# Optimization experiments

Hardware: AMD Instinct MI355X
Metric: run time of the kernel (lower is better)

## Reference

```python
import jax, jax.numpy as jnp
import numpy as np
import math

D_MODEL, HEADS, KQ = 1024, 16, 64
B, S = 2, 2048

def setup_inputs() -> dict:
    key = jax.random.key(0)
    k1, k2, k3, k4, k5 = jax.random.split(key, 5)
    scale = D_MODEL ** (-0.5)
    return {
        "x_BSE": jax.random.normal(k1, (B, S, D_MODEL), dtype=jnp.float32),
        "w_q": jax.random.normal(k2, (D_MODEL, HEADS, KQ), dtype=jnp.float32) * scale,
        "w_k": jax.random.normal(k3, (D_MODEL, HEADS, KQ), dtype=jnp.float32) * scale,
        "w_v": jax.random.normal(k4, (D_MODEL, HEADS, KQ), dtype=jnp.float32) * scale,
        "w_o": jax.random.normal(k5, (D_MODEL, HEADS, KQ), dtype=jnp.float32) * scale,
    }

def reference(x_BSE, w_q, w_k, w_v, w_o):
    # QKV projections (self-attention: memory = x)
    q_BSHK = jnp.einsum('BSE,EHK->BSHK', x_BSE, w_q)
    k_BMHK = jnp.einsum('BSE,EHK->BSHK', x_BSE, w_k)
    v_BMHK = jnp.einsum('BSE,EHK->BSHK', x_BSE, w_v)
    logits_BSHM = jnp.einsum('BSHK,BMHK->BSHM', q_BSHK, k_BMHK) / math.sqrt(KQ)
    # causal (diagonal) mask: query position >= memory position
    Sdim, Mdim = logits_BSHM.shape[1], logits_BSHM.shape[3]
    qpos = jnp.arange(Sdim)[:, None]          # [S,1]
    mpos = jnp.arange(Mdim)[None, :]          # [1,M]
    mask_SM = jnp.where(qpos >= mpos, 0.0, -jnp.inf).astype(logits_BSHM.dtype)
    logits_BSHM = logits_BSHM + mask_SM[None, :, None, :]
    probs_BSHM = jax.nn.softmax(logits_BSHM, axis=3)
    out_BSHK = jnp.einsum('BSHM,BMHK->BSHK', probs_BSHM, v_BMHK)
    return jnp.einsum('BSHK,EHK->BSE', out_BSHK, w_o)
```

## Files before the change

### kernel.cpp

```cpp
#include <hip/hip_runtime.h>
#include <hip/hip_bf16.h>

typedef __attribute__((ext_vector_type(4)))  float f32x4;
typedef __attribute__((ext_vector_type(16))) float f32x16;
typedef __attribute__((ext_vector_type(8)))  short short8;
typedef __attribute__((ext_vector_type(4)))  short short4v;

__device__ __forceinline__ short f2bf(float f) {
  union { float f; unsigned u; } x; x.f = f;
  unsigned r = (x.u + 0x7FFFu + ((x.u >> 16) & 1u)) >> 16;
  return (short)r;
}
__device__ __forceinline__ unsigned cvtpk(float lo, float hi) {
  unsigned r;
  asm("v_cvt_pk_bf16_f32 %0, %1, %2" : "=v"(r) : "v"(lo), "v"(hi));
  return r;
}

__global__ __launch_bounds__(256) void k_cast(const float* __restrict__ in,
                                              short* __restrict__ out, int n4) {
  int i = blockIdx.x * 256 + threadIdx.x;
  if (i >= n4) return;
  f32x4 v = ((const f32x4*)in)[i];
  short4v s;
  s[0] = f2bf(v[0]); s[1] = f2bf(v[1]); s[2] = f2bf(v[2]); s[3] = f2bf(v[3]);
  ((short4v*)out)[i] = s;
}

__global__ __launch_bounds__(256) void k_pack(const float* __restrict__ wq,
                                              const float* __restrict__ wk,
                                              const float* __restrict__ wv,
                                              short* __restrict__ WT) {
  int nt = blockIdx.x, et = blockIdx.y, sel = blockIdx.z;
  const float* w = sel == 0 ? wq : (sel == 1 ? wk : wv);
  __shared__ float tile[64][65];
  int tid = threadIdx.x;
  int cl = tid & 63, rw = tid >> 6;
#pragma unroll
  for (int j = 0; j < 16; ++j) {
    int el = j * 4 + rw;
    tile[el][cl] = w[(size_t)(et * 64 + el) * 1024 + nt * 64 + cl];
  }
  __syncthreads();
#pragma unroll
  for (int j = 0; j < 16; ++j) {
    int nl = j * 4 + rw;
    int n = sel * 1024 + nt * 64 + nl;
    WT[(size_t)n * 1024 + et * 64 + cl] = f2bf(tile[cl][nl]);
  }
}

template <int EPI>
__global__ __launch_bounds__(256) void k_gemm(const short* __restrict__ A,
                                              const short* __restrict__ B,
                                              short* __restrict__ Qo, short* __restrict__ Ko,
                                              short* __restrict__ Vo, float* __restrict__ out,
                                              int M, int N, int K) {
  __shared__ short As[128][40];
  __shared__ short Bs[128][40];
  int tid = threadIdx.x;
  int bm = blockIdx.y * 128, bn = blockIdx.x * 128;
  int wid = tid >> 6, lane = tid & 63;
  int wm = (wid >> 1) * 64, wn = (wid & 1) * 64;
  int lg = lane >> 4, lr = lane & 15;
  f32x4 acc[4][4] = {};

  int sr = tid >> 2, sc = tid & 3;
  const short* Ar0 = A + (size_t)(bm + sr) * K;
  const short* Ar1 = A + (size_t)(bm + sr + 64) * K;
  const short* Br0 = B + (size_t)(bn + sr) * K;
  const short* Br1 = B + (size_t)(bn + sr + 64) * K;

  short8 pa0 = *(const short8*)&Ar0[sc * 8];
  short8 pa1 = *(const short8*)&Ar1[sc * 8];
  short8 pb0 = *(const short8*)&Br0[sc * 8];
  short8 pb1 = *(const short8*)&Br1[sc * 8];

  int nk = K >> 5;
  for (int kt = 0; kt < nk; ++kt) {
    __syncthreads();
    *(short8*)&As[sr][sc * 8] = pa0;
    *(short8*)&As[sr + 64][sc * 8] = pa1;
    *(short8*)&Bs[sr][sc * 8] = pb0;
    *(short8*)&Bs[sr + 64][sc * 8] = pb1;
    if (kt + 1 < nk) {
      int ko = (kt + 1) * 32;
      pa0 = *(const short8*)&Ar0[ko + sc * 8];
      pa1 = *(const short8*)&Ar1[ko + sc * 8];
      pb0 = *(const short8*)&Br0[ko + sc * 8];
      pb1 = *(const short8*)&Br1[ko + sc * 8];
    }
    __syncthreads();
    short8 af[4], bf_[4];
#pragma unroll
    for (int mt = 0; mt < 4; ++mt)
      af[mt] = *(const short8*)&As[wm + mt * 16 + lr][lg * 8];
#pragma unroll
    for (int ntl = 0; ntl < 4; ++ntl)
      bf_[ntl] = *(const short8*)&Bs[wn + ntl * 16 + lr][lg * 8];
#pragma unroll
    for (int mt = 0; mt < 4; ++mt)
#pragma unroll
      for (int ntl = 0; ntl < 4; ++ntl)
        acc[mt][ntl] = __builtin_amdgcn_mfma_f32_16x16x32_bf16(af[mt], bf_[ntl], acc[mt][ntl], 0, 0, 0);
  }

#pragma unroll
  for (int mt = 0; mt < 4; ++mt)
#pragma unroll
    for (int ntl = 0; ntl < 4; ++ntl) {
      int m0 = bm + wm + mt * 16 + lg * 4;
      int n = bn + wn + ntl * 16 + lr;
      if (EPI == 0) {
        int b = m0 >> 11, s0 = m0 & 2047;
        int sel = n >> 10, hk = n & 1023;
        int h = hk >> 6, kd = hk & 63;
        if (sel == 0) {
#pragma unroll
          for (int rr = 0; rr < 4; ++rr)
            Qo[((size_t)(b * 16 + h) * 2048 + s0 + rr) * 64 + kd] =
                f2bf(acc[mt][ntl][rr] * 0.18033688011112042f);
        } else if (sel == 1) {
#pragma unroll
          for (int rr = 0; rr < 4; ++rr)
            Ko[((size_t)(b * 16 + h) * 2048 + s0 + rr) * 64 + kd] = f2bf(acc[mt][ntl][rr]);
        } else {
          short4v v4;
#pragma unroll
          for (int rr = 0; rr < 4; ++rr) v4[rr] = f2bf(acc[mt][ntl][rr]);
          *(short4v*)&Vo[((size_t)(b * 16 + h) * 64 + kd) * 2048 + s0] = v4;
        }
      } else {
#pragma unroll
        for (int rr = 0; rr < 4; ++rr)
          out[(size_t)(m0 + rr) * 1024 + n] = acc[mt][ntl][rr];
      }
    }
}

__global__ __launch_bounds__(128, 2) void k_attn(const short* __restrict__ Q,
                                                 const short* __restrict__ K,
                                                 const short* __restrict__ VT,
                                                 short* __restrict__ O) {
  const int S = 2048;
  int bh = blockIdx.x;
  int g = 31 - blockIdx.y;

  int tid = threadIdx.x;
  int wid = tid >> 6, lane = tid & 63;
  int hi = lane >> 5, ln = lane & 31;
  int qw = 2 * g + wid;
  int q_g = qw * 32 + ln;
  int npair = g + 1;

  __shared__ short Ks[2][2][32][64];
  __shared__ short Vs[2][2][64][32];

  const short* Qb = Q + (size_t)bh * S * 64;
  const short* Kb = K + (size_t)bh * S * 64;
  const short* Vb = VT + (size_t)bh * 64 * S;

  short8 qf[4];
#pragma unroll
  for (int ds = 0; ds < 4; ++ds)
    qf[ds] = *(const short8*)&Qb[(size_t)q_g * 64 + ds * 16 + hi * 8];

  int kr = tid >> 2, kcb = tid & 3;
  int vd = tid >> 1, vcb = tid & 1;
  const short* kgp = Kb + (size_t)kr * 64;
  const short* vgp = Vb + (size_t)vd * S;

  short8 ka0 = *(const short8*)&kgp[kcb * 8];
  short8 ka1 = *(const short8*)&kgp[(kcb + 4) * 8];
  short8 kb0 = *(const short8*)&kgp[2048 + kcb * 8];
  short8 kb1 = *(const short8*)&kgp[2048 + (kcb + 4) * 8];
  short8 va0 = *(const short8*)&vgp[vcb * 8];
  short8 va1 = *(const short8*)&vgp[(vcb + 2) * 8];
  short8 vb0 = *(const short8*)&vgp[32 + vcb * 8];
  short8 vb1 = *(const short8*)&vgp[32 + (vcb + 2) * 8];

  f32x16 acoA = {}, acoB = {};
  float l = 0.f;

  for (int p = 0; p < npair; ++p) {
    int pb = p & 1;
    *(short8*)&Ks[pb][0][kr][(kcb ^ (kr & 7)) * 8]       = ka0;
    *(short8*)&Ks[pb][0][kr][((kcb + 4) ^ (kr & 7)) * 8] = ka1;
    *(short8*)&Ks[pb][1][kr][(kcb ^ (kr & 7)) * 8]       = kb0;
    *(short8*)&Ks[pb][1][kr][((kcb + 4) ^ (kr & 7)) * 8] = kb1;
    *(short8*)&Vs[pb][0][vd][(vcb ^ (vd & 3)) * 8]       = va0;
    *(short8*)&Vs[pb][0][vd][((vcb + 2) ^ (vd & 3)) * 8] = va1;
    *(short8*)&Vs[pb][1][vd][(vcb ^ (vd & 3)) * 8]       = vb0;
    *(short8*)&Vs[pb][1][vd][((vcb + 2) ^ (vd & 3)) * 8] = vb1;
    if (p + 1 < npair) {
      size_t ko0 = (size_t)(2 * p + 2) * 2048, ko1 = (size_t)(2 * p + 3) * 2048;
      size_t vo0 = (size_t)(2 * p + 2) * 32,   vo1 = (size_t)(2 * p + 3) * 32;
      ka0 = *(const short8*)&kgp[ko0 + kcb * 8];
      ka1 = *(const short8*)&kgp[ko0 + (kcb + 4) * 8];
      kb0 = *(const short8*)&kgp[ko1 + kcb * 8];
      kb1 = *(const short8*)&kgp[ko1 + (kcb + 4) * 8];
      va0 = *(const short8*)&vgp[vo0 + vcb * 8];
      va1 = *(const short8*)&vgp[vo0 + (vcb + 2) * 8];
      vb0 = *(const short8*)&vgp[vo1 + vcb * 8];
      vb1 = *(const short8*)&vgp[vo1 + (vcb + 2) * 8];
    }
    __syncthreads();

    int t0 = 2 * p, t1 = 2 * p + 1;

    short8 kc00 = *(const short8*)&Ks[pb][0][ln][((0 + hi) ^ (ln & 7)) * 8];
    short8 kc01 = *(const short8*)&Ks[pb][0][ln][((2 + hi) ^ (ln & 7)) * 8];
    short8 kc02 = *(const short8*)&Ks[pb][0][ln][((4 + hi) ^ (ln & 7)) * 8];
    short8 kc03 = *(const short8*)&Ks[pb][0][ln][((6 + hi) ^ (ln & 7)) * 8];
    short8 kc10 = *(const short8*)&Ks[pb][1][ln][((0 + hi) ^ (ln & 7)) * 8];
    short8 kc11 = *(const short8*)&Ks[pb][1][ln][((2 + hi) ^ (ln & 7)) * 8];
    short8 kc12 = *(const short8*)&Ks[pb][1][ln][((4 + hi) ^ (ln & 7)) * 8];
    short8 kc13 = *(const short8*)&Ks[pb][1][ln][((6 + hi) ^ (ln & 7)) * 8];

    f32x16 sa0 = {}, sa1 = {};
    __builtin_amdgcn_s_setprio(1);
    sa0 = __builtin_amdgcn_mfma_f32_32x32x16_bf16(kc00, qf[0], sa0, 0, 0, 0);
    sa1 = __builtin_amdgcn_mfma_f32_32x32x16_bf16(kc10, qf[0], sa1, 0, 0, 0);
    sa0 = __builtin_amdgcn_mfma_f32_32x32x16_bf16(kc01, qf[1], sa0, 0, 0, 0);
    sa1 = __builtin_amdgcn_mfma_f32_32x32x16_bf16(kc11, qf[1], sa1, 0, 0, 0);
    sa0 = __builtin_amdgcn_mfma_f32_32x32x16_bf16(kc02, qf[2], sa0, 0, 0, 0);
    sa1 = __builtin_amdgcn_mfma_f32_32x32x16_bf16(kc12, qf[2], sa1, 0, 0, 0);
    sa0 = __builtin_amdgcn_mfma_f32_32x32x16_bf16(kc03, qf[3], sa0, 0, 0, 0);
    sa1 = __builtin_amdgcn_mfma_f32_32x32x16_bf16(kc13, qf[3], sa1, 0, 0, 0);
    __builtin_amdgcn_s_setprio(0);

    if (t0 >= qw) {
#pragma unroll
      for (int r = 0; r < 16; ++r) {
        int kv_g = t0 * 32 + (r & 3) + 8 * (r >> 2) + 4 * hi;
        if (kv_g > q_g) sa0[r] = -1e30f;
      }
    }
    if (t1 >= qw) {
#pragma unroll
      for (int r = 0; r < 16; ++r) {
        int kv_g = t1 * 32 + (r & 3) + 8 * (r >> 2) + 4 * hi;
        if (kv_g > q_g) sa1[r] = -1e30f;
      }
    }

    float p0[16], p1[16];
#pragma unroll
    for (int r = 0; r < 16; ++r) p0[r] = exp2f(sa0[r]);
#pragma unroll
    for (int r = 0; r < 16; ++r) p1[r] = exp2f(sa1[r]);
    {
      float s00 = (p0[0] + p0[1]) + (p0[2] + p0[3]);
      float s01 = (p0[4] + p0[5]) + (p0[6] + p0[7]);
      float s02 = (p0[8] + p0[9]) + (p0[10] + p0[11]);
      float s03 = (p0[12] + p0[13]) + (p0[14] + p0[15]);
      float s10 = (p1[0] + p1[1]) + (p1[2] + p1[3]);
      float s11 = (p1[4] + p1[5]) + (p1[6] + p1[7]);
      float s12 = (p1[8] + p1[9]) + (p1[10] + p1[11]);
      float s13 = (p1[12] + p1[13]) + (p1[14] + p1[15]);
      l += ((s00 + s01) + (s02 + s03)) + ((s10 + s11) + (s12 + s13));
    }

    {
      short8 v00 = *(const short8*)&Vs[pb][0][ln][((0 + hi) ^ (ln & 3)) * 8];
      short8 v01 = *(const short8*)&Vs[pb][0][ln][((2 + hi) ^ (ln & 3)) * 8];
      short8 v10 = *(const short8*)&Vs[pb][0][32 + ln][((0 + hi) ^ (ln & 3)) * 8];
      short8 v11 = *(const short8*)&Vs[pb][0][32 + ln][((2 + hi) ^ (ln & 3)) * 8];
#pragma unroll
      for (int s = 0; s < 2; ++s) {
        unsigned c0 = cvtpk(p0[8 * s + 0], p0[8 * s + 1]);
        unsigned c1 = cvtpk(p0[8 * s + 2], p0[8 * s + 3]);
        unsigned c2 = cvtpk(p0[8 * s + 4], p0[8 * s + 5]);
        unsigned c3 = cvtpk(p0[8 * s + 6], p0[8 * s + 7]);
        unsigned r1 = (unsigned)__shfl_xor((int)(hi ? c0 : c2), 32);
        unsigned r2 = (unsigned)__shfl_xor((int)(hi ? c1 : c3), 32);
        union { unsigned u[4]; short8 v; } pbv;
        pbv.u[0] = hi ? r1 : c0;
        pbv.u[1] = hi ? r2 : c1;
        pbv.u[2] = hi ? c2 : r1;
        pbv.u[3] = hi ? c3 : r2;
        __builtin_amdgcn_s_setprio(1);
        if (s == 0) {
          acoA = __builtin_amdgcn_mfma_f32_32x32x16_bf16(v00, pbv.v, acoA, 0, 0, 0);
          acoB = __builtin_amdgcn_mfma_f32_32x32x16_bf16(v10, pbv.v, acoB, 0, 0, 0);
        } else {
          acoA = __builtin_amdgcn_mfma_f32_32x32x16_bf16(v01, pbv.v, acoA, 0, 0, 0);
          acoB = __builtin_amdgcn_mfma_f32_32x32x16_bf16(v11, pbv.v, acoB, 0, 0, 0);
        }
        __builtin_amdgcn_s_setprio(0);
      }
    }
    {
      short8 v00 = *(const short8*)&Vs[pb][1][ln][((0 + hi) ^ (ln & 3)) * 8];
      short8 v01 = *(const short8*)&Vs[pb][1][ln][((2 + hi) ^ (ln & 3)) * 8];
      short8 v10 = *(const short8*)&Vs[pb][1][32 + ln][((0 + hi) ^ (ln & 3)) * 8];
      short8 v11 = *(const short8*)&Vs[pb][1][32 + ln][((2 + hi) ^ (ln & 3)) * 8];
#pragma unroll
      for (int s = 0; s < 2; ++s) {
        unsigned c0 = cvtpk(p1[8 * s + 0], p1[8 * s + 1]);
        unsigned c1 = cvtpk(p1[8 * s + 2], p1[8 * s + 3]);
        unsigned c2 = cvtpk(p1[8 * s + 4], p1[8 * s + 5]);
        unsigned c3 = cvtpk(p1[8 * s + 6], p1[8 * s + 7]);
        unsigned r1 = (unsigned)__shfl_xor((int)(hi ? c0 : c2), 32);
        unsigned r2 = (unsigned)__shfl_xor((int)(hi ? c1 : c3), 32);
        union { unsigned u[4]; short8 v; } pbv;
        pbv.u[0] = hi ? r1 : c0;
        pbv.u[1] = hi ? r2 : c1;
        pbv.u[2] = hi ? c2 : r1;
        pbv.u[3] = hi ? c3 : r2;
        __builtin_amdgcn_s_setprio(1);
        if (s == 0) {
          acoA = __builtin_amdgcn_mfma_f32_32x32x16_bf16(v00, pbv.v, acoA, 0, 0, 0);
          acoB = __builtin_amdgcn_mfma_f32_32x32x16_bf16(v10, pbv.v, acoB, 0, 0, 0);
        } else {
          acoA = __builtin_amdgcn_mfma_f32_32x32x16_bf16(v01, pbv.v, acoA, 0, 0, 0);
          acoB = __builtin_amdgcn_mfma_f32_32x32x16_bf16(v11, pbv.v, acoB, 0, 0, 0);
        }
        __builtin_amdgcn_s_setprio(0);
      }
    }
  }

  l += __shfl_xor(l, 32);
  float rl = 1.f / l;
  int b = bh >> 4, h = bh & 15;
  size_t obase = ((size_t)b * 2048 + q_g) * 1024 + h * 64;
#pragma unroll
  for (int g4 = 0; g4 < 4; ++g4) {
    int d0 = 8 * g4 + 4 * hi;
    *(unsigned*)&O[obase + d0]          = cvtpk(acoA[4 * g4] * rl, acoA[4 * g4 + 1] * rl);
    *(unsigned*)&O[obase + d0 + 2]      = cvtpk(acoA[4 * g4 + 2] * rl, acoA[4 * g4 + 3] * rl);
    *(unsigned*)&O[obase + 32 + d0]     = cvtpk(acoB[4 * g4] * rl, acoB[4 * g4 + 1] * rl);
    *(unsigned*)&O[obase + 32 + d0 + 2] = cvtpk(acoB[4 * g4 + 2] * rl, acoB[4 * g4 + 3] * rl);
  }
}

extern "C" void kernel_launch(void* const* d_in, const int* in_sizes, int n_in,
                              void* d_out, int out_size, void* d_ws, size_t ws_size,
                              hipStream_t stream) {
  const float* x  = (const float*)d_in[0];
  const float* wq = (const float*)d_in[1];
  const float* wk = (const float*)d_in[2];
  const float* wv = (const float*)d_in[3];
  const float* wo = (const float*)d_in[4];
  float* out = (float*)d_out;
  char* ws = (char*)d_ws;

  short* x_bf  = (short*)(ws);
  short* WqkvT = (short*)(ws + ((size_t)8 << 20));
  short* wo_bf = (short*)(ws + ((size_t)14 << 20));
  short* Qb    = (short*)(ws + ((size_t)16 << 20));
  short* Kb    = (short*)(ws + ((size_t)24 << 20));
  short* Vt    = (short*)(ws + ((size_t)32 << 20));
  short* Ob    = (short*)(ws + ((size_t)40 << 20));

  k_cast<<<4096, 256, 0, stream>>>(x, x_bf, 1048576);
  k_cast<<<1024, 256, 0, stream>>>(wo, wo_bf, 262144);
  k_pack<<<dim3(16, 16, 3), 256, 0, stream>>>(wq, wk, wv, WqkvT);
  k_gemm<0><<<dim3(24, 32), 256, 0, stream>>>(x_bf, WqkvT, Qb, Kb, Vt, nullptr, 4096, 3072, 1024);
  k_attn<<<dim3(32, 32), 128, 0, stream>>>(Qb, Kb, Vt, Ob);
  k_gemm<1><<<dim3(8, 32), 256, 0, stream>>>(Ob, wo_bf, nullptr, nullptr, nullptr, out, 4096, 1024, 1024);
}
```

Measured before the change: 124.7 us.

## Process two query tiles per attention wave to reuse staged K/V tiles

Each attention block now covers 128 query rows instead of 64, with each wave handling two 32-row query tiles that share the same K/V tiles in LDS. This halves the grid in y and halves global K/V traffic and LDS staging per query, and it hoists the V fragment reads out so both query sets use them. It also rewrites the P permutation to use four lane shuffles instead of two selected ones. In exchange the kernel uses more registers (two sets of accumulators and Q fragments), launches fewer blocks, and gives the diagonal block some masked work that is wasted.

```diff
diff --git a/kernel.cpp b/kernel.cpp
--- a/kernel.cpp
+++ b/kernel.cpp
@@ -144,14 +144,16 @@
                                                  short* __restrict__ O) {
   const int S = 2048;
   int bh = blockIdx.x;
-  int g = 31 - blockIdx.y;
+  int g = 15 - blockIdx.y;
 
   int tid = threadIdx.x;
   int wid = tid >> 6, lane = tid & 63;
   int hi = lane >> 5, ln = lane & 31;
-  int qw = 2 * g + wid;
-  int q_g = qw * 32 + ln;
-  int npair = g + 1;
+  int qw0 = 4 * g + 2 * wid;
+  int qw1 = qw0 + 1;
+  int q_g0 = qw0 * 32 + ln;
+  int q_g1 = q_g0 + 32;
+  int npair = 2 * g + 2;
 
   __shared__ short Ks[2][2][32][64];
   __shared__ short Vs[2][2][64][32];
@@ -160,10 +162,12 @@
   const short* Kb = K + (size_t)bh * S * 64;
   const short* Vb = VT + (size_t)bh * 64 * S;
 
-  short8 qf[4];
-#pragma unroll
-  for (int ds = 0; ds < 4; ++ds)
-    qf[ds] = *(const short8*)&Qb[(size_t)q_g * 64 + ds * 16 + hi * 8];
+  short8 qf0[4], qf1[4];
+#pragma unroll
+  for (int ds = 0; ds < 4; ++ds) {
+    qf0[ds] = *(const short8*)&Qb[(size_t)q_g0 * 64 + ds * 16 + hi * 8];
+    qf1[ds] = *(const short8*)&Qb[(size_t)q_g1 * 64 + ds * 16 + hi * 8];
+  }
 
   int kr = tid >> 2, kcb = tid & 3;
   int vd = tid >> 1, vcb = tid & 1;
@@ -179,8 +183,8 @@
   short8 vb0 = *(const short8*)&vgp[32 + vcb * 8];
   short8 vb1 = *(const short8*)&vgp[32 + (vcb + 2) * 8];
 
-  f32x16 acoA = {}, acoB = {};
-  float l = 0.f;
+  f32x16 acoA0 = {}, acoB0 = {}, acoA1 = {}, acoB1 = {};
+  float l0 = 0.f, l1 = 0.f;
 
   for (int p = 0; p < npair; ++p) {
     int pb = p & 1;
@@ -216,122 +220,133 @@
     short8 kc11 = *(const short8*)&Ks[pb][1][ln][((2 + hi) ^ (ln & 7)) * 8];
     short8 kc12 = *(const short8*)&Ks[pb][1][ln][((4 + hi) ^ (ln & 7)) * 8];
     short8 kc13 = *(const short8*)&Ks[pb][1][ln][((6 + hi) ^ (ln & 7)) * 8];
-
-    f32x16 sa0 = {}, sa1 = {};
-    __builtin_amdgcn_s_setprio(1);
-    sa0 = __builtin_amdgcn_mfma_f32_32x32x16_bf16(kc00, qf[0], sa0, 0, 0, 0);
-    sa1 = __builtin_amdgcn_mfma_f32_32x32x16_bf16(kc10, qf[0], sa1, 0, 0, 0);
-    sa0 = __builtin_amdgcn_mfma_f32_32x32x16_bf16(kc01, qf[1], sa0, 0, 0, 0);
-    sa1 = __builtin_amdgcn_mfma_f32_32x32x16_bf16(kc11, qf[1], sa1, 0, 0, 0);
-    sa0 = __builtin_amdgcn_mfma_f32_32x32x16_bf16(kc02, qf[2], sa0, 0, 0, 0);
-    sa1 = __builtin_amdgcn_mfma_f32_32x32x16_bf16(kc12, qf[2], sa1, 0, 0, 0);
-    sa0 = __builtin_amdgcn_mfma_f32_32x32x16_bf16(kc03, qf[3], sa0, 0, 0, 0);
-    sa1 = __builtin_amdgcn_mfma_f32_32x32x16_bf16(kc13, qf[3], sa1, 0, 0, 0);
-    __builtin_amdgcn_s_setprio(0);
-
-    if (t0 >= qw) {
-#pragma unroll
-      for (int r = 0; r < 16; ++r) {
-        int kv_g = t0 * 32 + (r & 3) + 8 * (r >> 2) + 4 * hi;
-        if (kv_g > q_g) sa0[r] = -1e30f;
-      }
+    short8 v000 = *(const short8*)&Vs[pb][0][ln][((0 + hi) ^ (ln & 3)) * 8];
+    short8 v001 = *(const short8*)&Vs[pb][0][ln][((2 + hi) ^ (ln & 3)) * 8];
+    short8 v010 = *(const short8*)&Vs[pb][0][32 + ln][((0 + hi) ^ (ln & 3)) * 8];
+    short8 v011 = *(const short8*)&Vs[pb][0][32 + ln][((2 + hi) ^ (ln & 3)) * 8];
+    short8 v100 = *(const short8*)&Vs[pb][1][ln][((0 + hi) ^ (ln & 3)) * 8];
+    short8 v101 = *(const short8*)&Vs[pb][1][ln][((2 + hi) ^ (ln & 3)) * 8];
+    short8 v110 = *(const short8*)&Vs[pb][1][32 + ln][((0 + hi) ^ (ln & 3)) * 8];
+    short8 v111 = *(const short8*)&Vs[pb][1][32 + ln][((2 + hi) ^ (ln & 3)) * 8];
+
+#define DO_QSET(QW, QG, QF, ACA, ACB, LV)                                       \
+    {                                                                           \
+      f32x16 sa0 = {}, sa1 = {};                                                \
+      __builtin_amdgcn_s_setprio(1);                                            \
+      sa0 = __builtin_amdgcn_mfma_f32_32x32x16_bf16(kc00, QF[0], sa0, 0, 0, 0); \
+      sa1 = __builtin_amdgcn_mfma_f32_32x32x16_bf16(kc10, QF[0], sa1, 0, 0, 0); \
+      sa0 = __builtin_amdgcn_mfma_f32_32x32x16_bf16(kc01, QF[1], sa0, 0, 0, 0); \
+      sa1 = __builtin_amdgcn_mfma_f32_32x32x16_bf16(kc11, QF[1], sa1, 0, 0, 0); \
+      sa0 = __builtin_amdgcn_mfma_f32_32x32x16_bf16(kc02, QF[2], sa0, 0, 0, 0); \
+      sa1 = __builtin_amdgcn_mfma_f32_32x32x16_bf16(kc12, QF[2], sa1, 0, 0, 0); \
+      sa0 = __builtin_amdgcn_mfma_f32_32x32x16_bf16(kc03, QF[3], sa0, 0, 0, 0); \
+      sa1 = __builtin_amdgcn_mfma_f32_32x32x16_bf16(kc13, QF[3], sa1, 0, 0, 0); \
+      __builtin_amdgcn_s_setprio(0);                                            \
+      if (t0 >= (QW)) {                                                         \
+        _Pragma("unroll")                                                       \
+        for (int r = 0; r < 16; ++r) {                                          \
+          int kv_g = t0 * 32 + (r & 3) + 8 * (r >> 2) + 4 * hi;                 \
+          if (kv_g > (QG)) sa0[r] = -1e30f;                                     \
+        }                                                                       \
+      }                                                                         \
+      if (t1 >= (QW)) {                                                         \
+        _Pragma("unroll")                                                       \
+        for (int r = 0; r < 16; ++r) {                                          \
+          int kv_g = t1 * 32 + (r & 3) + 8 * (r >> 2) + 4 * hi;                 \
+          if (kv_g > (QG)) sa1[r] = -1e30f;                                     \
+        }                                                                       \
+      }                                                                         \
+      float p0[16], p1[16];                                                     \
+      _Pragma("unroll")                                                         \
+      for (int r = 0; r < 16; ++r) p0[r] = exp2f(sa0[r]);                       \
+      _Pragma("unroll")                                                         \
+      for (int r = 0; r < 16; ++r) p1[r] = exp2f(sa1[r]);                       \
+      {                                                                         \
+        float s00 = (p0[0] + p0[1]) + (p0[2] + p0[3]);                          \
+        float s01 = (p0[4] + p0[5]) + (p0[6] + p0[7]);                          \
+        float s02 = (p0[8] + p0[9]) + (p0[10] + p0[11]);                        \
+        float s03 = (p0[12] + p0[13]) + (p0[14] + p0[15]);                      \
+        float s10 = (p1[0] + p1[1]) + (p1[2] + p1[3]);                          \
+        float s11 = (p1[4] + p1[5]) + (p1[6] + p1[7]);                          \
+        float s12 = (p1[8] + p1[9]) + (p1[10] + p1[11]);                        \
+        float s13 = (p1[12] + p1[13]) + (p1[14] + p1[15]);                      \
+        LV += ((s00 + s01) + (s02 + s03)) + ((s10 + s11) + (s12 + s13));        \
+      }                                                                         \
+      _Pragma("unroll")                                                         \
+      for (int s = 0; s < 2; ++s) {                                             \
+        unsigned c0 = cvtpk(p0[8 * s + 0], p0[8 * s + 1]);                      \
+        unsigned c1 = cvtpk(p0[8 * s + 2], p0[8 * s + 3]);                      \
+        unsigned c2 = cvtpk(p0[8 * s + 4], p0[8 * s + 5]);                      \
+        unsigned c3 = cvtpk(p0[8 * s + 6], p0[8 * s + 7]);                      \
+        unsigned pc0 = (unsigned)__shfl_xor((int)c0, 32);                       \
+        unsigned pc1 = (unsigned)__shfl_xor((int)c1, 32);                       \
+        unsigned pc2 = (unsigned)__shfl_xor((int)c2, 32);                       \
+        unsigned pc3 = (unsigned)__shfl_xor((int)c3, 32);                       \
+        union { unsigned u[4]; short8 v; } pbv;                                 \
+        pbv.u[0] = hi ? pc2 : c0;                                               \
+        pbv.u[1] = hi ? pc3 : c1;                                               \
+        pbv.u[2] = hi ? c2 : pc0;                                               \
+        pbv.u[3] = hi ? c3 : pc1;                                               \
+        __builtin_amdgcn_s_setprio(1);                                          \
+        if (s == 0) {                                                           \
+          ACA = __builtin_amdgcn_mfma_f32_32x32x16_bf16(v000, pbv.v, ACA, 0, 0, 0);\
+          ACB = __builtin_amdgcn_mfma_f32_32x32x16_bf16(v010, pbv.v, ACB, 0, 0, 0);\
+        } else {                                                                \
+          ACA = __builtin_amdgcn_mfma_f32_32x32x16_bf16(v001, pbv.v, ACA, 0, 0, 0);\
+          ACB = __builtin_amdgcn_mfma_f32_32x32x16_bf16(v011, pbv.v, ACB, 0, 0, 0);\
+        }                                                                       \
+        __builtin_amdgcn_s_setprio(0);                                          \
+      }                                                                         \
+      _Pragma("unroll")                                                         \
+      for (int s = 0; s < 2; ++s) {                                             \
+        unsigned c0 = cvtpk(p1[8 * s + 0], p1[8 * s + 1]);                      \
+        unsigned c1 = cvtpk(p1[8 * s + 2], p1[8 * s + 3]);                      \
+        unsigned c2 = cvtpk(p1[8 * s + 4], p1[8 * s + 5]);                      \
+        unsigned c3 = cvtpk(p1[8 * s + 6], p1[8 * s + 7]);                      \
+        unsigned pc0 = (unsigned)__shfl_xor((int)c0, 32);                       \
+        unsigned pc1 = (unsigned)__shfl_xor((int)c1, 32);                       \
+        unsigned pc2 = (unsigned)__shfl_xor((int)c2, 32);                       \
+        unsigned pc3 = (unsigned)__shfl_xor((int)c3, 32);                       \
+        union { unsigned u[4]; short8 v; } pbv;                                 \
+        pbv.u[0] = hi ? pc2 : c0;                                               \
+        pbv.u[1] = hi ? pc3 : c1;                                               \
+        pbv.u[2] = hi ? c2 : pc0;                                               \
+        pbv.u[3] = hi ? c3 : pc1;                                               \
+        __builtin_amdgcn_s_setprio(1);                                          \
+        if (s == 0) {                                                           \
+          ACA = __builtin_amdgcn_mfma_f32_32x32x16_bf16(v100, pbv.v, ACA, 0, 0, 0);\
+          ACB = __builtin_amdgcn_mfma_f32_32x32x16_bf16(v110, pbv.v, ACB, 0, 0, 0);\
+        } else {                                                                \
+          ACA = __builtin_amdgcn_mfma_f32_32x32x16_bf16(v101, pbv.v, ACA, 0, 0, 0);\
+          ACB = __builtin_amdgcn_mfma_f32_32x32x16_bf16(v111, pbv.v, ACB, 0, 0, 0);\
+        }                                                                       \
+        __builtin_amdgcn_s_setprio(0);                                          \
+      }                                                                         \
     }
-    if (t1 >= qw) {
-#pragma unroll
-      for (int r = 0; r < 16; ++r) {
-        int kv_g = t1 * 32 + (r & 3) + 8 * (r >> 2) + 4 * hi;
-        if (kv_g > q_g) sa1[r] = -1e30f;
-      }
-    }
-
-    float p0[16], p1[16];
-#pragma unroll
-    for (int r = 0; r < 16; ++r) p0[r] = exp2f(sa0[r]);
-#pragma unroll
-    for (int r = 0; r < 16; ++r) p1[r] = exp2f(sa1[r]);
-    {
-      float s00 = (p0[0] + p0[1]) + (p0[2] + p0[3]);
-      float s01 = (p0[4] + p0[5]) + (p0[6] + p0[7]);
-      float s02 = (p0[8] + p0[9]) + (p0[10] + p0[11]);
-      float s03 = (p0[12] + p0[13]) + (p0[14] + p0[15]);
-      float s10 = (p1[0] + p1[1]) + (p1[2] + p1[3]);
-      float s11 = (p1[4] + p1[5]) + (p1[6] + p1[7]);
-      float s12 = (p1[8] + p1[9]) + (p1[10] + p1[11]);
-      float s13 = (p1[12] + p1[13]) + (p1[14] + p1[15]);
-      l += ((s00 + s01) + (s02 + s03)) + ((s10 + s11) + (s12 + s13));
-    }
-
-    {
-      short8 v00 = *(const short8*)&Vs[pb][0][ln][((0 + hi) ^ (ln & 3)) * 8];
-      short8 v01 = *(const short8*)&Vs[pb][0][ln][((2 + hi) ^ (ln & 3)) * 8];
-      short8 v10 = *(const short8*)&Vs[pb][0][32 + ln][((0 + hi) ^ (ln & 3)) * 8];
-      short8 v11 = *(const short8*)&Vs[pb][0][32 + ln][((2 + hi) ^ (ln & 3)) * 8];
-#pragma unroll
-      for (int s = 0; s < 2; ++s) {
-        unsigned c0 = cvtpk(p0[8 * s + 0], p0[8 * s + 1]);
-        unsigned c1 = cvtpk(p0[8 * s + 2], p0[8 * s + 3]);
-        unsigned c2 = cvtpk(p0[8 * s + 4], p0[8 * s + 5]);
-        unsigned c3 = cvtpk(p0[8 * s + 6], p0[8 * s + 7]);
-        unsigned r1 = (unsigned)__shfl_xor((int)(hi ? c0 : c2), 32);
-        unsigned r2 = (unsigned)__shfl_xor((int)(hi ? c1 : c3), 32);
-        union { unsigned u[4]; short8 v; } pbv;
-        pbv.u[0] = hi ? r1 : c0;
-        pbv.u[1] = hi ? r2 : c1;
-        pbv.u[2] = hi ? c2 : r1;
-        pbv.u[3] = hi ? c3 : r2;
-        __builtin_amdgcn_s_setprio(1);
-        if (s == 0) {
-          acoA = __builtin_amdgcn_mfma_f32_32x32x16_bf16(v00, pbv.v, acoA, 0, 0, 0);
-          acoB = __builtin_amdgcn_mfma_f32_32x32x16_bf16(v10, pbv.v, acoB, 0, 0, 0);
-        } else {
-          acoA = __builtin_amdgcn_mfma_f32_32x32x16_bf16(v01, pbv.v, acoA, 0, 0, 0);
-          acoB = __builtin_amdgcn_mfma_f32_32x32x16_bf16(v11, pbv.v, acoB, 0, 0, 0);
-        }
-        __builtin_amdgcn_s_setprio(0);
-      }
-    }
-    {
-      short8 v00 = *(const short8*)&Vs[pb][1][ln][((0 + hi) ^ (ln & 3)) * 8];
-      short8 v01 = *(const short8*)&Vs[pb][1][ln][((2 + hi) ^ (ln & 3)) * 8];
-      short8 v10 = *(const short8*)&Vs[pb][1][32 + ln][((0 + hi) ^ (ln & 3)) * 8];
-      short8 v11 = *(const short8*)&Vs[pb][1][32 + ln][((2 + hi) ^ (ln & 3)) * 8];
-#pragma unroll
-      for (int s = 0; s < 2; ++s) {
-        unsigned c0 = cvtpk(p1[8 * s + 0], p1[8 * s + 1]);
-        unsigned c1 = cvtpk(p1[8 * s + 2], p1[8 * s + 3]);
-        unsigned c2 = cvtpk(p1[8 * s + 4], p1[8 * s + 5]);
-        unsigned c3 = cvtpk(p1[8 * s + 6], p1[8 * s + 7]);
-        unsigned r1 = (unsigned)__shfl_xor((int)(hi ? c0 : c2), 32);
-        unsigned r2 = (unsigned)__shfl_xor((int)(hi ? c1 : c3), 32);
-        union { unsigned u[4]; short8 v; } pbv;
-        pbv.u[0] = hi ? r1 : c0;
-        pbv.u[1] = hi ? r2 : c1;
-        pbv.u[2] = hi ? c2 : r1;
-        pbv.u[3] = hi ? c3 : r2;
-        __builtin_amdgcn_s_setprio(1);
-        if (s == 0) {
-          acoA = __builtin_amdgcn_mfma_f32_32x32x16_bf16(v00, pbv.v, acoA, 0, 0, 0);
-          acoB = __builtin_amdgcn_mfma_f32_32x32x16_bf16(v10, pbv.v, acoB, 0, 0, 0);
-        } else {
-          acoA = __builtin_amdgcn_mfma_f32_32x32x16_bf16(v01, pbv.v, acoA, 0, 0, 0);
-          acoB = __builtin_amdgcn_mfma_f32_32x32x16_bf16(v11, pbv.v, acoB, 0, 0, 0);
-        }
-        __builtin_amdgcn_s_setprio(0);
-      }
-    }
-  }
-
-  l += __shfl_xor(l, 32);
-  float rl = 1.f / l;
+
+    DO_QSET(qw0, q_g0, qf0, acoA0, acoB0, l0)
+    DO_QSET(qw1, q_g1, qf1, acoA1, acoB1, l1)
+#undef DO_QSET
+  }
+
   int b = bh >> 4, h = bh & 15;
-  size_t obase = ((size_t)b * 2048 + q_g) * 1024 + h * 64;
+  l0 += __shfl_xor(l0, 32);
+  l1 += __shfl_xor(l1, 32);
+  float rl0 = 1.f / l0;
+  float rl1 = 1.f / l1;
+  size_t ob0 = ((size_t)b * 2048 + q_g0) * 1024 + h * 64;
+  size_t ob1 = ((size_t)b * 2048 + q_g1) * 1024 + h * 64;
 #pragma unroll
   for (int g4 = 0; g4 < 4; ++g4) {
     int d0 = 8 * g4 + 4 * hi;
-    *(unsigned*)&O[obase + d0]          = cvtpk(acoA[4 * g4] * rl, acoA[4 * g4 + 1] * rl);
-    *(unsigned*)&O[obase + d0 + 2]      = cvtpk(acoA[4 * g4 + 2] * rl, acoA[4 * g4 + 3] * rl);
-    *(unsigned*)&O[obase + 32 + d0]     = cvtpk(acoB[4 * g4] * rl, acoB[4 * g4 + 1] * rl);
-    *(unsigned*)&O[obase + 32 + d0 + 2] = cvtpk(acoB[4 * g4 + 2] * rl, acoB[4 * g4 + 3] * rl);
+    *(unsigned*)&O[ob0 + d0]          = cvtpk(acoA0[4 * g4] * rl0, acoA0[4 * g4 + 1] * rl0);
+    *(unsigned*)&O[ob0 + d0 + 2]      = cvtpk(acoA0[4 * g4 + 2] * rl0, acoA0[4 * g4 + 3] * rl0);
+    *(unsigned*)&O[ob0 + 32 + d0]     = cvtpk(acoB0[4 * g4] * rl0, acoB0[4 * g4 + 1] * rl0);
+    *(unsigned*)&O[ob0 + 32 + d0 + 2] = cvtpk(acoB0[4 * g4 + 2] * rl0, acoB0[4 * g4 + 3] * rl0);
+    *(unsigned*)&O[ob1 + d0]          = cvtpk(acoA1[4 * g4] * rl1, acoA1[4 * g4 + 1] * rl1);
+    *(unsigned*)&O[ob1 + d0 + 2]      = cvtpk(acoA1[4 * g4 + 2] * rl1, acoA1[4 * g4 + 3] * rl1);
+    *(unsigned*)&O[ob1 + 32 + d0]     = cvtpk(acoB1[4 * g4] * rl1, acoB1[4 * g4 + 1] * rl1);
+    *(unsigned*)&O[ob1 + 32 + d0 + 2] = cvtpk(acoB1[4 * g4 + 2] * rl1, acoB1[4 * g4 + 3] * rl1);
   }
 }
 
@@ -358,6 +373,6 @@
   k_cast<<<1024, 256, 0, stream>>>(wo, wo_bf, 262144);
   k_pack<<<dim3(16, 16, 3), 256, 0, stream>>>(wq, wk, wv, WqkvT);
   k_gemm<0><<<dim3(24, 32), 256, 0, stream>>>(x_bf, WqkvT, Qb, Kb, Vt, nullptr, 4096, 3072, 1024);
-  k_attn<<<dim3(32, 32), 128, 0, stream>>>(Qb, Kb, Vt, Ob);
+  k_attn<<<dim3(32, 16), 128, 0, stream>>>(Qb, Kb, Vt, Ob);
   k_gemm<1><<<dim3(8, 32), 256, 0, stream>>>(Ob, wo_bf, nullptr, nullptr, nullptr, out, 4096, 1024, 1024);
 }
```

Result: slower. 203.3 us (+63.0%).
